# Kernel optimization log

Hardware: AMD Instinct MI355X
Metric: run time of the kernel (lower is better)

The kernel has to match this reference:

```python
import jax, jax.numpy as jnp
import numpy as np

E = 8
HIDDEN = 1024
INTER = 4096
CAPS = np.array([512, 1024, 2048, 4096, 1024, 512, 2048, 1024], dtype=np.int64)  # sum = 12288
TOTAL = int(CAPS.sum())


def setup_inputs() -> dict:
    key = jax.random.key(0)
    k1, k2, k3, k4, k5 = jax.random.split(key, 5)
    s1 = 1.0 / np.sqrt(HIDDEN)
    s2 = 1.0 / np.sqrt(INTER)
    return {
        "inter_state": jax.random.normal(k1, (TOTAL, HIDDEN), dtype=jnp.float32),
        "w1": jax.random.normal(k2, (E, INTER, HIDDEN), dtype=jnp.float32) * s1,
        "b1": jax.random.normal(k3, (E, INTER), dtype=jnp.float32) * s1,
        "w2": jax.random.normal(k4, (E, HIDDEN, INTER), dtype=jnp.float32) * s2,
        "b2": jax.random.normal(k5, (E, HIDDEN), dtype=jnp.float32) * s2,
        "capacities": jnp.asarray(CAPS),
    }


def reference(inter_state, w1, b1, w2, b2, capacities):
    # Grouped GEMM: tokens are contiguous per expert with sizes = capacities.
    # Capacities are routing metadata (static for slicing).
    caps = np.asarray(capacities)
    offs = np.concatenate([[0], np.cumsum(caps)]).astype(np.int64)
    outs = []
    for e in range(caps.shape[0]):  # small fixed expert loop
        x = inter_state[int(offs[e]):int(offs[e + 1])]      # [cap_e, hidden]
        h = x @ w1[e].T + b1[e]                              # [cap_e, inter]
        outs.append(h @ w2[e].T + b2[e])                     # [cap_e, hidden]
    return jnp.concatenate(outs, axis=0)                     # [total, hidden]
```

## Files before the change

kernel.cpp:

```cpp
#include <hip/hip_runtime.h>
#include <hip/hip_bf16.h>

#define DEV __device__ __forceinline__

typedef __bf16 bf16x8 __attribute__((ext_vector_type(8)));
typedef float  f32x4  __attribute__((ext_vector_type(4)));


DEV unsigned short f2bf(float f) {
  union { float f; unsigned u; } v; v.f = f;
  unsigned u = v.u;
  return (unsigned short)((u + 0x7FFFu + ((u >> 16) & 1u)) >> 16);
}

DEV void gld_lds16(const void* g, void* l) {
  __builtin_amdgcn_global_load_lds(
      (const __attribute__((address_space(1))) unsigned int*)g,
      (__attribute__((address_space(3))) unsigned int*)l, 16, 0, 0);
}

#define WAITVM(N) asm volatile("s_waitcnt vmcnt(" #N ")" ::: "memory"); \
                  __builtin_amdgcn_sched_barrier(0)
#define WAITLG(N) asm volatile("s_waitcnt lgkmcnt(" #N ")" ::: "memory"); \
                  __builtin_amdgcn_sched_barrier(0)

template <int K_, int N_, bool OUT_BF16, bool HAS_BIAS, int EDIV>
__global__ __launch_bounds__(512, 2)
void gemm8(const unsigned short* __restrict__ A,
           const unsigned short* __restrict__ B,
           const float* __restrict__ bias, void* __restrict__ Cv) {
  __shared__ __align__(128) char lds[2][49152];

  const int t    = threadIdx.x;
  const int lane = t & 63;
  const int wv   = t >> 6;
  const int wm   = wv >> 1;
  const int wn   = wv & 1;
  const int fr   = lane & 15;
  const int fq   = lane >> 4;

  constexpr int NCT = N_ / 128;
  constexpr int NT  = K_ / 64;

  int bid = blockIdx.x;
  const int nwg = gridDim.x;
  bid = (bid & 7) * (nwg >> 3) + (bid >> 3);

  const int rt = bid / NCT;
  const int ct = bid - rt * NCT;

  int e;
  if constexpr (EDIV > 0) {
    e = rt / EDIV;
  } else {
    const int cums[9] = {0, 2, 6, 14, 30, 34, 36, 44, 48};
    e = 0;
#pragma unroll
    for (int i = 1; i < 8; ++i) e += (rt >= cums[i]) ? 1 : 0;
  }

  const int grow0 = rt * 256;
  const int nloc0 = ct * 128;
  const unsigned short* Bg = B + (size_t)e * N_ * K_;

  f32x4 acc[4][4];
#pragma unroll
  for (int i = 0; i < 4; ++i)
#pragma unroll
    for (int j = 0; j < 4; ++j) acc[i][j] = (f32x4){0.f, 0.f, 0.f, 0.f};

  auto stage = [&](int buf, int tk) {
    const int kb = tk * 64;
    char* Abase = lds[buf];
    char* Bbase = lds[buf] + 32768;
#pragma unroll
    for (int s = 0; s < 4; ++s) {
      int o  = s * 8192 + wv * 1024 + lane * 16;
      int r  = o >> 7;
      int cb = (o & 127) ^ ((r & 7) << 4);
      gld_lds16(A + (size_t)(grow0 + r) * K_ + kb + (cb >> 1),
                Abase + s * 8192 + wv * 1024);
    }
#pragma unroll
    for (int s = 0; s < 2; ++s) {
      int o  = s * 8192 + wv * 1024 + lane * 16;
      int r  = o >> 7;
      int cb = (o & 127) ^ ((r & 7) << 4);
      gld_lds16(Bg + (size_t)(nloc0 + r) * K_ + kb + (cb >> 1),
                Bbase + s * 8192 + wv * 1024);
    }
  };

  stage(0, 0);
  for (int tk = 0; tk < NT; ++tk) {
    const int cur = tk & 1;
    if (tk + 1 < NT) {
      stage(cur ^ 1, tk + 1);
      WAITVM(6);
    } else {
      WAITVM(0);
    }
    __builtin_amdgcn_s_barrier();

    char* Abase = lds[cur];
    char* Bbase = lds[cur] + 32768;
    bf16x8 af[4][2], bf[4][2];
#pragma unroll
    for (int mi = 0; mi < 2; ++mi) {
      int r = wm * 64 + mi * 16 + fr;
#pragma unroll
      for (int k = 0; k < 2; ++k)
        af[mi][k] = *(bf16x8*)(Abase + r * 128 + ((k * 64 + fq * 16) ^ ((r & 7) << 4)));
    }
#pragma unroll
    for (int ni = 0; ni < 4; ++ni) {
      int r = wn * 64 + ni * 16 + fr;
#pragma unroll
      for (int k = 0; k < 2; ++k)
        bf[ni][k] = *(bf16x8*)(Bbase + r * 128 + ((k * 64 + fq * 16) ^ ((r & 7) << 4)));
    }
    __builtin_amdgcn_sched_barrier(0);
#pragma unroll
    for (int mi = 2; mi < 4; ++mi) {
      int r = wm * 64 + mi * 16 + fr;
#pragma unroll
      for (int k = 0; k < 2; ++k)
        af[mi][k] = *(bf16x8*)(Abase + r * 128 + ((k * 64 + fq * 16) ^ ((r & 7) << 4)));
    }
    WAITLG(4);
    __builtin_amdgcn_s_setprio(1);
#pragma unroll
    for (int k = 0; k < 2; ++k)
#pragma unroll
      for (int mi = 0; mi < 2; ++mi)
#pragma unroll
        for (int ni = 0; ni < 4; ++ni)
          acc[mi][ni] = __builtin_amdgcn_mfma_f32_16x16x32_bf16(
              af[mi][k], bf[ni][k], acc[mi][ni], 0, 0, 0);
    __builtin_amdgcn_s_setprio(0);
    WAITLG(0);
    __builtin_amdgcn_s_setprio(1);
#pragma unroll
    for (int k = 0; k < 2; ++k)
#pragma unroll
      for (int mi = 2; mi < 4; ++mi)
#pragma unroll
        for (int ni = 0; ni < 4; ++ni)
          acc[mi][ni] = __builtin_amdgcn_mfma_f32_16x16x32_bf16(
              af[mi][k], bf[ni][k], acc[mi][ni], 0, 0, 0);
    __builtin_amdgcn_s_setprio(0);
    __builtin_amdgcn_s_barrier();
  }

#pragma unroll
  for (int ni = 0; ni < 4; ++ni) {
    int nloc = nloc0 + wn * 64 + ni * 16 + fr;
    float bv = 0.f;
    if constexpr (HAS_BIAS) bv = (bias + (size_t)e * N_)[nloc];
#pragma unroll
    for (int mi = 0; mi < 4; ++mi) {
      int m = grow0 + wm * 64 + mi * 16 + fq * 4;
#pragma unroll
      for (int j = 0; j < 4; ++j) {
        float val = acc[mi][ni][j] + bv;
        if constexpr (OUT_BF16)
          ((unsigned short*)Cv)[(size_t)(m + j) * N_ + nloc] = f2bf(val);
        else
          ((float*)Cv)[(size_t)(m + j) * N_ + nloc] = val;
      }
    }
  }
}

DEV int swz(int r, int cbyte) {
  return (r * 64 + cbyte) ^ (((r >> 1) & 7) << 4);
}

template <int K_, int N_, int NCT_, int AMODE, int BMODE, bool OUT_BF16,
          bool HAS_BIAS, int EDIV>
__global__ __launch_bounds__(256)
void gemm_expert(const void* __restrict__ Av, const void* __restrict__ Bv,
                 const float* __restrict__ bias, void* __restrict__ Cv) {
  __shared__ char lds[2][12288];

  const int t    = threadIdx.x;
  const int lane = t & 63;
  const int wv   = t >> 6;
  const int wr   = wv >> 1;
  const int wc   = wv & 1;
  const int fr   = lane & 15;
  const int fq   = lane >> 4;

  int bid = blockIdx.x;
  const int nwg = gridDim.x;
  if ((nwg & 7) == 0) bid = (bid & 7) * (nwg >> 3) + (bid >> 3);

  const int rt = bid / NCT_;
  const int ct = bid - rt * NCT_;

  int e;
  if constexpr (EDIV > 0) {
    e = rt / EDIV;
  } else {
    const int cums[9] = {0, 4, 12, 28, 60, 68, 72, 88, 96};
    e = 0;
#pragma unroll
    for (int i = 1; i < 8; ++i) e += (rt >= cums[i]) ? 1 : 0;
  }

  const int grow0 = rt * 128;
  const int nloc0 = ct * 64;

  f32x4 acc[4][2];
#pragma unroll
  for (int i = 0; i < 4; ++i)
#pragma unroll
    for (int j = 0; j < 2; ++j) acc[i][j] = (f32x4){0.f, 0.f, 0.f, 0.f};

  const unsigned short* Ab = (const unsigned short*)Av;
  const float*          Af = (const float*)Av;
  const unsigned short* Bb = (const unsigned short*)Bv + (size_t)e * N_ * K_;
  const float*          Bf = (const float*)Bv + (size_t)e * N_ * K_;

  auto stage = [&](int buf, int kb) {
    char* As = lds[buf];
    char* Bs = lds[buf] + 8192;
    if constexpr (AMODE == 1) {
#pragma unroll
      for (int s = 0; s < 2; ++s) {
        int o = (wv * 2 + s) * 1024 + lane * 16;
        int p = o ^ (((o >> 7) & 7) << 4);
        gld_lds16(Ab + (size_t)(grow0 + (p >> 6)) * K_ + kb + ((p & 63) >> 1),
                  As + (wv * 2 + s) * 1024);
      }
    } else {
#pragma unroll
      for (int it = 0; it < 4; ++it) {
        int q = t + it * 256, r = q >> 3, c = (q & 7) * 4;
        float4 f = *(const float4*)(Af + (size_t)(grow0 + r) * K_ + kb + c);
        ushort4 v = {f2bf(f.x), f2bf(f.y), f2bf(f.z), f2bf(f.w)};
        *(ushort4*)(As + swz(r, c * 2)) = v;
      }
    }
    if constexpr (BMODE == 1) {
      int o = wv * 1024 + lane * 16;
      int p = o ^ (((o >> 7) & 7) << 4);
      gld_lds16(Bb + (size_t)(nloc0 + (p >> 6)) * K_ + kb + ((p & 63) >> 1),
                Bs + wv * 1024);
    } else {
#pragma unroll
      for (int it = 0; it < 2; ++it) {
        int q = t + it * 256, r = q >> 3, c = (q & 7) * 4;
        float4 f = *(const float4*)(Bf + (size_t)(nloc0 + r) * K_ + kb + c);
        ushort4 v = {f2bf(f.x), f2bf(f.y), f2bf(f.z), f2bf(f.w)};
        *(ushort4*)(Bs + swz(r, c * 2)) = v;
      }
    }
  };

  auto compute = [&](int buf) {
    char* As = lds[buf];
    char* Bs = lds[buf] + 8192;
    bf16x8 af[4], bfg[2];
#pragma unroll
    for (int mi = 0; mi < 4; ++mi)
      af[mi] = *(bf16x8*)(As + swz(wr * 64 + mi * 16 + fr, fq * 16));
#pragma unroll
    for (int ni = 0; ni < 2; ++ni)
      bfg[ni] = *(bf16x8*)(Bs + swz(wc * 32 + ni * 16 + fr, fq * 16));
#pragma unroll
    for (int mi = 0; mi < 4; ++mi)
#pragma unroll
      for (int ni = 0; ni < 2; ++ni)
        acc[mi][ni] = __builtin_amdgcn_mfma_f32_16x16x32_bf16(
            af[mi], bfg[ni], acc[mi][ni], 0, 0, 0);
  };

  int cur = 0;
  stage(0, 0);
  __syncthreads();
#pragma unroll 2
  for (int kb = 32; kb < K_; kb += 32) {
    stage(cur ^ 1, kb);
    compute(cur);
    __syncthreads();
    cur ^= 1;
  }
  compute(cur);

#pragma unroll
  for (int ni = 0; ni < 2; ++ni) {
    int nloc = nloc0 + wc * 32 + ni * 16 + fr;
    float bv = 0.f;
    if constexpr (HAS_BIAS) bv = (bias + (size_t)e * N_)[nloc];
#pragma unroll
    for (int mi = 0; mi < 4; ++mi) {
      int m = grow0 + wr * 64 + mi * 16 + fq * 4;
#pragma unroll
      for (int j = 0; j < 4; ++j) {
        float val = acc[mi][ni][j] + bv;
        if constexpr (OUT_BF16)
          ((unsigned short*)Cv)[(size_t)(m + j) * N_ + nloc] = f2bf(val);
        else
          ((float*)Cv)[(size_t)(m + j) * N_ + nloc] = val;
      }
    }
  }
}

__global__ __launch_bounds__(256)
void transpose_w1(const float* __restrict__ w1, unsigned short* __restrict__ w1t) {
  __shared__ unsigned short tl[64 * 68];
  int b = blockIdx.x;
  int jt = b & 15, kt = (b >> 4) & 63, e = b >> 10;
  const float* src = w1 + ((size_t)e * 4096 + kt * 64) * 1024 + jt * 64;
  int t = threadIdx.x;
#pragma unroll
  for (int it = 0; it < 4; ++it) {
    int q = t + it * 256, kr = q >> 4, jc = (q & 15) * 4;
    float4 f = *(const float4*)(src + (size_t)kr * 1024 + jc);
    ushort4 v = {f2bf(f.x), f2bf(f.y), f2bf(f.z), f2bf(f.w)};
    *(ushort4*)&tl[kr * 68 + jc] = v;
  }
  __syncthreads();
  unsigned short* dst = w1t + ((size_t)e * 1024 + jt * 64) * 4096 + kt * 64;
#pragma unroll
  for (int it = 0; it < 4; ++it) {
    int q = t + it * 256, jr = q >> 4, kc = (q & 15) * 4;
    ushort4 v = {tl[(kc + 0) * 68 + jr], tl[(kc + 1) * 68 + jr],
                 tl[(kc + 2) * 68 + jr], tl[(kc + 3) * 68 + jr]};
    *(ushort4*)(dst + (size_t)jr * 4096 + kc) = v;
  }
}

template <bool STORE_BF>
__global__ __launch_bounds__(256)
void conv_w2_bias(const float* __restrict__ w2, const float* __restrict__ b1,
                  const float* __restrict__ b2, unsigned short* __restrict__ w2bf,
                  float* __restrict__ bc) {
  int row = blockIdx.x, e = row >> 10, t = threadIdx.x;
  const float* src = w2 + (size_t)row * 4096;
  const float* b1e = b1 + (size_t)e * 4096;
  float acc = 0.f;
#pragma unroll
  for (int it = 0; it < 4; ++it) {
    int c = (t + it * 256) * 4;
    float4 f = *(const float4*)(src + c);
    float4 g = *(const float4*)(b1e + c);
    acc += f.x * g.x + f.y * g.y + f.z * g.z + f.w * g.w;
    if constexpr (STORE_BF) {
      ushort4 v = {f2bf(f.x), f2bf(f.y), f2bf(f.z), f2bf(f.w)};
      *(ushort4*)(w2bf + (size_t)row * 4096 + c) = v;
    }
  }
#pragma unroll
  for (int o = 32; o > 0; o >>= 1) acc += __shfl_down(acc, o);
  __shared__ float red[4];
  if ((t & 63) == 0) red[t >> 6] = acc;
  __syncthreads();
  if (t == 0) bc[row] = red[0] + red[1] + red[2] + red[3] + b2[row];
}

__global__ __launch_bounds__(256)
void conv_f32_bf16(const float* __restrict__ in, unsigned short* __restrict__ out,
                   int n4) {
  for (int i = blockIdx.x * 256 + threadIdx.x; i < n4; i += gridDim.x * 256) {
    float4 f = *(const float4*)(in + (size_t)i * 4);
    ushort4 v = {f2bf(f.x), f2bf(f.y), f2bf(f.z), f2bf(f.w)};
    *(ushort4*)(out + (size_t)i * 4) = v;
  }
}

extern "C" void kernel_launch(void* const* d_in, const int* in_sizes, int n_in,
                              void* d_out, int out_size, void* d_ws, size_t ws_size,
                              hipStream_t stream) {
  const float* x  = (const float*)d_in[0];
  const float* w1 = (const float*)d_in[1];
  const float* b1 = (const float*)d_in[2];
  const float* w2 = (const float*)d_in[3];
  const float* b2 = (const float*)d_in[4];

  char* ws = (char*)d_ws;
  unsigned short* w1t = (unsigned short*)ws;
  const size_t NEED_T2 = 151126016, NEED_T3 = 176291840;

  if (ws_size >= NEED_T2) {
    unsigned short* w2bf = (unsigned short*)(ws + 67108864);
    unsigned short* Wc   = (unsigned short*)(ws + 134217728);
    float*          bc   = (float*)(ws + 150994944);

    transpose_w1<<<8192, 256, 0, stream>>>(w1, w1t);
    conv_w2_bias<true><<<8192, 256, 0, stream>>>(w2, b1, b2, w2bf, bc);
    gemm8<4096, 1024, true, false, 4>
        <<<256, 512, 0, stream>>>(w2bf, w1t, nullptr, Wc);
    if (ws_size >= NEED_T3) {
      unsigned short* xbf = (unsigned short*)(ws + 151126016);
      conv_f32_bf16<<<2048, 256, 0, stream>>>(x, xbf, 12288 * 1024 / 4);
      gemm8<1024, 1024, false, true, 0>
          <<<384, 512, 0, stream>>>(xbf, Wc, bc, (float*)d_out);
    } else {
      gemm_expert<1024, 1024, 16, 0, 1, false, true, 0>
          <<<1536, 256, 0, stream>>>(x, Wc, bc, d_out);
    }
  } else {
    unsigned short* Wc = (unsigned short*)(ws + 67108864);
    float*          bc = (float*)(ws + 83886080);

    transpose_w1<<<8192, 256, 0, stream>>>(w1, w1t);
    conv_w2_bias<false><<<8192, 256, 0, stream>>>(w2, b1, b2, nullptr, bc);
    gemm_expert<4096, 1024, 16, 0, 1, true, false, 8>
        <<<1024, 256, 0, stream>>>(w2, w1t, nullptr, Wc);
    gemm_expert<1024, 1024, 16, 0, 1, false, true, 0>
        <<<1536, 256, 0, stream>>>(x, Wc, bc, d_out);
  }
}
```

Baseline: 204.2 us.

## Add 256x256-tile GEMM with split-K for the weight-combine stage

Adds a new gemm256 kernel with 256x256 output tiles. Its next-tile loads are staged in halves, interleaved with the MFMA phases. The W2·W1 combine GEMM now runs as a two-way split-K whose partial results go into the unused xbf buffer, and a new reduce_bf16 kernel sums them. The token GEMM also moves to gemm256 with 192 blocks, so fewer blocks run than the GPU has compute units, and the split-K adds an extra reduction pass and a second bf16 rounding. The older gemm8 compute is folded into a lambda with a single LDS wait, and the fallback paths are trimmed.

```diff
diff --git a/kernel.cpp b/kernel.cpp
--- a/kernel.cpp
+++ b/kernel.cpp
@@ -13,6 +13,10 @@
   return (unsigned short)((u + 0x7FFFu + ((u >> 16) & 1u)) >> 16);
 }
 
+DEV float bf2f(unsigned short s) {
+  union { unsigned u; float f; } v; v.u = (unsigned)s << 16; return v.f;
+}
+
 DEV void gld_lds16(const void* g, void* l) {
   __builtin_amdgcn_global_load_lds(
       (const __attribute__((address_space(1))) unsigned int*)g,
@@ -23,6 +27,184 @@
                   __builtin_amdgcn_sched_barrier(0)
 #define WAITLG(N) asm volatile("s_waitcnt lgkmcnt(" #N ")" ::: "memory"); \
                   __builtin_amdgcn_sched_barrier(0)
+
+template <int KT_, int KLEN, int SK, int N_, int NCT, bool OUT_BF16,
+          bool HAS_BIAS, int EDIV>
+__global__ __launch_bounds__(512, 2)
+void gemm256(const unsigned short* __restrict__ A,
+             const unsigned short* __restrict__ B,
+             const float* __restrict__ bias,
+             void* __restrict__ C0, void* __restrict__ C1) {
+  __shared__ __align__(128) char lds[2][65536];
+  constexpr int NTILES = KLEN / 64;
+
+  const int tid  = threadIdx.x;
+  const int lane = tid & 63;
+  const int wv   = tid >> 6;
+  const int wm   = wv >> 2;
+  const int wn   = wv & 3;
+  const int fr   = lane & 15;
+  const int fq   = lane >> 4;
+
+  int bid = blockIdx.x;
+  const int nwg = gridDim.x;
+  bid = (bid & 7) * (nwg >> 3) + (bid >> 3);
+
+  int sk = 0;
+  if constexpr (SK > 1) {
+    const int per = nwg / SK;
+    sk = bid / per;
+    bid -= sk * per;
+  }
+  const int kStart = sk * KLEN;
+  void* Cv = (SK > 1 && sk == 1) ? C1 : C0;
+
+  const int rt = bid / NCT;
+  const int ct = bid - rt * NCT;
+
+  int e;
+  if constexpr (EDIV > 0) {
+    e = rt / EDIV;
+  } else {
+    const int cums[9] = {0, 2, 6, 14, 30, 34, 36, 44, 48};
+    e = 0;
+#pragma unroll
+    for (int i = 1; i < 8; ++i) e += (rt >= cums[i]) ? 1 : 0;
+  }
+
+  const int grow0 = rt * 256;
+  const int nloc0 = ct * 256;
+  const unsigned short* Bg = B + (size_t)e * N_ * KT_;
+
+  f32x4 acc[8][4];
+#pragma unroll
+  for (int i = 0; i < 8; ++i)
+#pragma unroll
+    for (int j = 0; j < 4; ++j) acc[i][j] = (f32x4){0.f, 0.f, 0.f, 0.f};
+
+  auto stage_half = [&](int buf, int tk2, int h) {
+    const int kb = kStart + tk2 * 64;
+    char* dst = lds[buf] + h * 16384;
+    const unsigned short* src = (h < 2) ? A : Bg;
+    const int row0 = (h < 2) ? (grow0 + h * 128) : (nloc0 + (h - 2) * 128);
+#pragma unroll
+    for (int s = 0; s < 2; ++s) {
+      int o  = s * 8192 + wv * 1024 + lane * 16;
+      int r  = o >> 7;
+      int cb = (o & 127) ^ ((r & 7) << 4);
+      gld_lds16(src + (size_t)(row0 + r) * KT_ + kb + (cb >> 1),
+                dst + s * 8192 + wv * 1024);
+    }
+  };
+
+  stage_half(0, 0, 0); stage_half(0, 0, 1);
+  stage_half(0, 0, 2); stage_half(0, 0, 3);
+
+  const int brow0 = (wn & 1) * 64;
+
+  for (int tk = 0; tk < NTILES; ++tk) {
+    const int cur = tk & 1;
+    WAITVM(0);
+    __builtin_amdgcn_s_barrier();
+    __builtin_amdgcn_sched_barrier(0);
+
+    char* Ah = lds[cur] + wm * 16384;
+    char* Bh = lds[cur] + (2 + (wn >> 1)) * 16384;
+    const bool pre = (tk + 1 < NTILES);
+
+    bf16x8 bfr[4][2], afr[2][2];
+#pragma unroll
+    for (int ni = 0; ni < 4; ++ni) {
+      int r = brow0 + ni * 16 + fr;
+#pragma unroll
+      for (int k = 0; k < 2; ++k)
+        bfr[ni][k] = *(bf16x8*)(Bh + r * 128 + ((k * 64 + fq * 16) ^ ((r & 7) << 4)));
+    }
+#pragma unroll
+    for (int j = 0; j < 2; ++j) {
+      int r = j * 16 + fr;
+#pragma unroll
+      for (int k = 0; k < 2; ++k)
+        afr[j][k] = *(bf16x8*)(Ah + r * 128 + ((k * 64 + fq * 16) ^ ((r & 7) << 4)));
+    }
+    if (pre) { stage_half(cur ^ 1, tk + 1, 0); stage_half(cur ^ 1, tk + 1, 1); }
+    WAITLG(0);
+    __builtin_amdgcn_s_setprio(1);
+#pragma unroll
+    for (int k = 0; k < 2; ++k)
+#pragma unroll
+      for (int j = 0; j < 2; ++j)
+#pragma unroll
+        for (int ni = 0; ni < 4; ++ni)
+          acc[j][ni] = __builtin_amdgcn_mfma_f32_16x16x32_bf16(
+              afr[j][k], bfr[ni][k], acc[j][ni], 0, 0, 0);
+    __builtin_amdgcn_s_setprio(0);
+
+#pragma unroll
+    for (int q = 1; q < 4; ++q) {
+#pragma unroll
+      for (int j = 0; j < 2; ++j) {
+        int r = (2 * q + j) * 16 + fr;
+#pragma unroll
+        for (int k = 0; k < 2; ++k)
+          afr[j][k] = *(bf16x8*)(Ah + r * 128 + ((k * 64 + fq * 16) ^ ((r & 7) << 4)));
+      }
+      if (q == 1 && pre) { stage_half(cur ^ 1, tk + 1, 2); stage_half(cur ^ 1, tk + 1, 3); }
+      WAITLG(0);
+      __builtin_amdgcn_s_setprio(1);
+#pragma unroll
+      for (int k = 0; k < 2; ++k)
+#pragma unroll
+        for (int j = 0; j < 2; ++j)
+#pragma unroll
+          for (int ni = 0; ni < 4; ++ni)
+            acc[2 * q + j][ni] = __builtin_amdgcn_mfma_f32_16x16x32_bf16(
+                afr[j][k], bfr[ni][k], acc[2 * q + j][ni], 0, 0, 0);
+      __builtin_amdgcn_s_setprio(0);
+    }
+  }
+
+#pragma unroll
+  for (int ni = 0; ni < 4; ++ni) {
+    int ncol = nloc0 + wn * 64 + ni * 16 + fr;
+    float bv = 0.f;
+    if constexpr (HAS_BIAS) bv = (bias + (size_t)e * N_)[ncol];
+#pragma unroll
+    for (int mi = 0; mi < 8; ++mi) {
+      int m = grow0 + wm * 128 + mi * 16 + fq * 4;
+#pragma unroll
+      for (int j = 0; j < 4; ++j) {
+        float val = acc[mi][ni][j] + bv;
+        if constexpr (OUT_BF16)
+          ((unsigned short*)Cv)[(size_t)(m + j) * N_ + ncol] = f2bf(val);
+        else
+          ((float*)Cv)[(size_t)(m + j) * N_ + ncol] = val;
+      }
+    }
+  }
+}
+
+__global__ __launch_bounds__(256)
+void reduce_bf16(const unsigned short* __restrict__ p0,
+                 const unsigned short* __restrict__ p1,
+                 unsigned short* __restrict__ out, int n8) {
+  for (int i = blockIdx.x * 256 + threadIdx.x; i < n8; i += gridDim.x * 256) {
+    ushort4 a0 = ((const ushort4*)p0)[2 * i];
+    ushort4 a1 = ((const ushort4*)p0)[2 * i + 1];
+    ushort4 b0 = ((const ushort4*)p1)[2 * i];
+    ushort4 b1 = ((const ushort4*)p1)[2 * i + 1];
+    ushort4 r0 = {f2bf(bf2f(a0.x) + bf2f(b0.x)), f2bf(bf2f(a0.y) + bf2f(b0.y)),
+                  f2bf(bf2f(a0.z) + bf2f(b0.z)), f2bf(bf2f(a0.w) + bf2f(b0.w))};
+    ushort4 r1 = {f2bf(bf2f(a1.x) + bf2f(b1.x)), f2bf(bf2f(a1.y) + bf2f(b1.y)),
+                  f2bf(bf2f(a1.z) + bf2f(b1.z)), f2bf(bf2f(a1.w) + bf2f(b1.w))};
+    ((ushort4*)out)[2 * i]     = r0;
+    ((ushort4*)out)[2 * i + 1] = r1;
+  }
+}
+
+DEV int swz(int r, int cbyte) {
+  return (r * 64 + cbyte) ^ (((r >> 1) & 7) << 4);
+}
 
 template <int K_, int N_, bool OUT_BF16, bool HAS_BIAS, int EDIV>
 __global__ __launch_bounds__(512, 2)
@@ -30,7 +212,6 @@
            const unsigned short* __restrict__ B,
            const float* __restrict__ bias, void* __restrict__ Cv) {
   __shared__ __align__(128) char lds[2][49152];
-
   const int t    = threadIdx.x;
   const int lane = t & 63;
   const int wv   = t >> 6;
@@ -38,14 +219,12 @@
   const int wn   = wv & 1;
   const int fr   = lane & 15;
   const int fq   = lane >> 4;
-
   constexpr int NCT = N_ / 128;
   constexpr int NT  = K_ / 64;
 
   int bid = blockIdx.x;
   const int nwg = gridDim.x;
   bid = (bid & 7) * (nwg >> 3) + (bid >> 3);
-
   const int rt = bid / NCT;
   const int ct = bid - rt * NCT;
 
@@ -89,6 +268,36 @@
       gld_lds16(Bg + (size_t)(nloc0 + r) * K_ + kb + (cb >> 1),
                 Bbase + s * 8192 + wv * 1024);
     }
+  };
+
+  auto compute = [&](int buf) {
+    char* Abase = lds[buf];
+    char* Bbase = lds[buf] + 32768;
+    bf16x8 af[4][2], bf[4][2];
+#pragma unroll
+    for (int mi = 0; mi < 4; ++mi) {
+      int r = wm * 64 + mi * 16 + fr;
+#pragma unroll
+      for (int k = 0; k < 2; ++k)
+        af[mi][k] = *(bf16x8*)(Abase + r * 128 + ((k * 64 + fq * 16) ^ ((r & 7) << 4)));
+    }
+#pragma unroll
+    for (int ni = 0; ni < 4; ++ni) {
+      int r = wn * 64 + ni * 16 + fr;
+#pragma unroll
+      for (int k = 0; k < 2; ++k)
+        bf[ni][k] = *(bf16x8*)(Bbase + r * 128 + ((k * 64 + fq * 16) ^ ((r & 7) << 4)));
+    }
+    __builtin_amdgcn_s_setprio(1);
+#pragma unroll
+    for (int k = 0; k < 2; ++k)
+#pragma unroll
+      for (int mi = 0; mi < 4; ++mi)
+#pragma unroll
+        for (int ni = 0; ni < 4; ++ni)
+          acc[mi][ni] = __builtin_amdgcn_mfma_f32_16x16x32_bf16(
+              af[mi][k], bf[ni][k], acc[mi][ni], 0, 0, 0);
+    __builtin_amdgcn_s_setprio(0);
   };
 
   stage(0, 0);
@@ -101,54 +310,8 @@
       WAITVM(0);
     }
     __builtin_amdgcn_s_barrier();
-
-    char* Abase = lds[cur];
-    char* Bbase = lds[cur] + 32768;
-    bf16x8 af[4][2], bf[4][2];
-#pragma unroll
-    for (int mi = 0; mi < 2; ++mi) {
-      int r = wm * 64 + mi * 16 + fr;
-#pragma unroll
-      for (int k = 0; k < 2; ++k)
-        af[mi][k] = *(bf16x8*)(Abase + r * 128 + ((k * 64 + fq * 16) ^ ((r & 7) << 4)));
-    }
-#pragma unroll
-    for (int ni = 0; ni < 4; ++ni) {
-      int r = wn * 64 + ni * 16 + fr;
-#pragma unroll
-      for (int k = 0; k < 2; ++k)
-        bf[ni][k] = *(bf16x8*)(Bbase + r * 128 + ((k * 64 + fq * 16) ^ ((r & 7) << 4)));
-    }
-    __builtin_amdgcn_sched_barrier(0);
-#pragma unroll
-    for (int mi = 2; mi < 4; ++mi) {
-      int r = wm * 64 + mi * 16 + fr;
-#pragma unroll
-      for (int k = 0; k < 2; ++k)
-        af[mi][k] = *(bf16x8*)(Abase + r * 128 + ((k * 64 + fq * 16) ^ ((r & 7) << 4)));
-    }
-    WAITLG(4);
-    __builtin_amdgcn_s_setprio(1);
-#pragma unroll
-    for (int k = 0; k < 2; ++k)
-#pragma unroll
-      for (int mi = 0; mi < 2; ++mi)
-#pragma unroll
-        for (int ni = 0; ni < 4; ++ni)
-          acc[mi][ni] = __builtin_amdgcn_mfma_f32_16x16x32_bf16(
-              af[mi][k], bf[ni][k], acc[mi][ni], 0, 0, 0);
-    __builtin_amdgcn_s_setprio(0);
+    compute(cur);
     WAITLG(0);
-    __builtin_amdgcn_s_setprio(1);
-#pragma unroll
-    for (int k = 0; k < 2; ++k)
-#pragma unroll
-      for (int mi = 2; mi < 4; ++mi)
-#pragma unroll
-        for (int ni = 0; ni < 4; ++ni)
-          acc[mi][ni] = __builtin_amdgcn_mfma_f32_16x16x32_bf16(
-              af[mi][k], bf[ni][k], acc[mi][ni], 0, 0, 0);
-    __builtin_amdgcn_s_setprio(0);
     __builtin_amdgcn_s_barrier();
   }
 
@@ -172,17 +335,11 @@
   }
 }
 
-DEV int swz(int r, int cbyte) {
-  return (r * 64 + cbyte) ^ (((r >> 1) & 7) << 4);
-}
-
-template <int K_, int N_, int NCT_, int AMODE, int BMODE, bool OUT_BF16,
-          bool HAS_BIAS, int EDIV>
+template <int K_, int N_, int NCT_, bool OUT_BF16, bool HAS_BIAS, int EDIV>
 __global__ __launch_bounds__(256)
 void gemm_expert(const void* __restrict__ Av, const void* __restrict__ Bv,
                  const float* __restrict__ bias, void* __restrict__ Cv) {
   __shared__ char lds[2][12288];
-
   const int t    = threadIdx.x;
   const int lane = t & 63;
   const int wv   = t >> 6;
@@ -194,7 +351,6 @@
   int bid = blockIdx.x;
   const int nwg = gridDim.x;
   if ((nwg & 7) == 0) bid = (bid & 7) * (nwg >> 3) + (bid >> 3);
-
   const int rt = bid / NCT_;
   const int ct = bid - rt * NCT_;
 
@@ -217,45 +373,23 @@
 #pragma unroll
     for (int j = 0; j < 2; ++j) acc[i][j] = (f32x4){0.f, 0.f, 0.f, 0.f};
 
-  const unsigned short* Ab = (const unsigned short*)Av;
-  const float*          Af = (const float*)Av;
+  const float* Af = (const float*)Av;
   const unsigned short* Bb = (const unsigned short*)Bv + (size_t)e * N_ * K_;
-  const float*          Bf = (const float*)Bv + (size_t)e * N_ * K_;
 
   auto stage = [&](int buf, int kb) {
     char* As = lds[buf];
     char* Bs = lds[buf] + 8192;
-    if constexpr (AMODE == 1) {
-#pragma unroll
-      for (int s = 0; s < 2; ++s) {
-        int o = (wv * 2 + s) * 1024 + lane * 16;
-        int p = o ^ (((o >> 7) & 7) << 4);
-        gld_lds16(Ab + (size_t)(grow0 + (p >> 6)) * K_ + kb + ((p & 63) >> 1),
-                  As + (wv * 2 + s) * 1024);
-      }
-    } else {
-#pragma unroll
-      for (int it = 0; it < 4; ++it) {
-        int q = t + it * 256, r = q >> 3, c = (q & 7) * 4;
-        float4 f = *(const float4*)(Af + (size_t)(grow0 + r) * K_ + kb + c);
-        ushort4 v = {f2bf(f.x), f2bf(f.y), f2bf(f.z), f2bf(f.w)};
-        *(ushort4*)(As + swz(r, c * 2)) = v;
-      }
-    }
-    if constexpr (BMODE == 1) {
-      int o = wv * 1024 + lane * 16;
-      int p = o ^ (((o >> 7) & 7) << 4);
-      gld_lds16(Bb + (size_t)(nloc0 + (p >> 6)) * K_ + kb + ((p & 63) >> 1),
-                Bs + wv * 1024);
-    } else {
-#pragma unroll
-      for (int it = 0; it < 2; ++it) {
-        int q = t + it * 256, r = q >> 3, c = (q & 7) * 4;
-        float4 f = *(const float4*)(Bf + (size_t)(nloc0 + r) * K_ + kb + c);
-        ushort4 v = {f2bf(f.x), f2bf(f.y), f2bf(f.z), f2bf(f.w)};
-        *(ushort4*)(Bs + swz(r, c * 2)) = v;
-      }
-    }
+#pragma unroll
+    for (int it = 0; it < 4; ++it) {
+      int q = t + it * 256, r = q >> 3, c = (q & 7) * 4;
+      float4 f = *(const float4*)(Af + (size_t)(grow0 + r) * K_ + kb + c);
+      ushort4 v = {f2bf(f.x), f2bf(f.y), f2bf(f.z), f2bf(f.w)};
+      *(ushort4*)(As + swz(r, c * 2)) = v;
+    }
+    int o = wv * 1024 + lane * 16;
+    int p = o ^ (((o >> 7) & 7) << 4);
+    gld_lds16(Bb + (size_t)(nloc0 + (p >> 6)) * K_ + kb + ((p & 63) >> 1),
+              Bs + wv * 1024);
   };
 
   auto compute = [&](int buf) {
@@ -279,7 +413,6 @@
   int cur = 0;
   stage(0, 0);
   __syncthreads();
-#pragma unroll 2
   for (int kb = 32; kb < K_; kb += 32) {
     stage(cur ^ 1, kb);
     compute(cur);
@@ -384,7 +517,22 @@
   unsigned short* w1t = (unsigned short*)ws;
   const size_t NEED_T2 = 151126016, NEED_T3 = 176291840;
 
-  if (ws_size >= NEED_T2) {
+  if (ws_size >= NEED_T3) {
+    unsigned short* w2bf = (unsigned short*)(ws + 67108864);
+    unsigned short* Wc   = (unsigned short*)(ws + 134217728);
+    float*          bc   = (float*)(ws + 150994944);
+    unsigned short* xbf  = (unsigned short*)(ws + 151126016);
+    unsigned short* p1   = xbf;
+
+    transpose_w1<<<8192, 256, 0, stream>>>(w1, w1t);
+    conv_w2_bias<true><<<8192, 256, 0, stream>>>(w2, b1, b2, w2bf, bc);
+    gemm256<4096, 2048, 2, 1024, 4, true, false, 4>
+        <<<256, 512, 0, stream>>>(w2bf, w1t, nullptr, Wc, p1);
+    reduce_bf16<<<2048, 256, 0, stream>>>(Wc, p1, Wc, 8 * 1024 * 1024 / 8);
+    conv_f32_bf16<<<2048, 256, 0, stream>>>(x, xbf, 12288 * 1024 / 4);
+    gemm256<1024, 1024, 1, 1024, 4, false, true, 0>
+        <<<192, 512, 0, stream>>>(xbf, Wc, bc, (float*)d_out, nullptr);
+  } else if (ws_size >= NEED_T2) {
     unsigned short* w2bf = (unsigned short*)(ws + 67108864);
     unsigned short* Wc   = (unsigned short*)(ws + 134217728);
     float*          bc   = (float*)(ws + 150994944);
@@ -393,24 +541,17 @@
     conv_w2_bias<true><<<8192, 256, 0, stream>>>(w2, b1, b2, w2bf, bc);
     gemm8<4096, 1024, true, false, 4>
         <<<256, 512, 0, stream>>>(w2bf, w1t, nullptr, Wc);
-    if (ws_size >= NEED_T3) {
-      unsigned short* xbf = (unsigned short*)(ws + 151126016);
-      conv_f32_bf16<<<2048, 256, 0, stream>>>(x, xbf, 12288 * 1024 / 4);
-      gemm8<1024, 1024, false, true, 0>
-          <<<384, 512, 0, stream>>>(xbf, Wc, bc, (float*)d_out);
-    } else {
-      gemm_expert<1024, 1024, 16, 0, 1, false, true, 0>
-          <<<1536, 256, 0, stream>>>(x, Wc, bc, d_out);
-    }
+    gemm_expert<1024, 1024, 16, false, true, 0>
+        <<<1536, 256, 0, stream>>>(x, Wc, bc, d_out);
   } else {
     unsigned short* Wc = (unsigned short*)(ws + 67108864);
     float*          bc = (float*)(ws + 83886080);
 
     transpose_w1<<<8192, 256, 0, stream>>>(w1, w1t);
     conv_w2_bias<false><<<8192, 256, 0, stream>>>(w2, b1, b2, nullptr, bc);
-    gemm_expert<4096, 1024, 16, 0, 1, true, false, 8>
-        <<<1024, 256, 0, stream>>>(w2, w1t, nullptr, Wc);
-    gemm_expert<1024, 1024, 16, 0, 1, false, true, 0>
+    gemm_expert<4096, 1024, 8, true, false, 8>
+        <<<768, 256, 0, stream>>>(w2, w1t, nullptr, Wc);
+    gemm_expert<1024, 1024, 16, false, true, 0>
         <<<1536, 256, 0, stream>>>(x, Wc, bc, d_out);
   }
 }
```

New measurement: 205.0 us. About the same (+0.4%).
